# Optimization experiments

Measured on AMD Instinct MI355X. Metric: run time of the kernel, lower is better.

Reference implementation:

```python
import jax, jax.numpy as jnp
import numpy as np

N = 100000
E = 1_600_000
EPS = 1e-5
NEG_SLOPE = 0.01


def leaky_relu(x):
    return jnp.where(x > 0, x, NEG_SLOPE * x)


def batchnorm(x, gamma, beta):
    # BatchNorm1d in training mode: batch statistics, biased variance
    m = jnp.mean(x, axis=0)
    v = jnp.mean((x - m) ** 2, axis=0)
    return (x - m) * jax.lax.rsqrt(v + EPS) * gamma + beta


def gcn_conv(x, W, b, src, dst, norm, n):
    # PyG GCNConv: h = x @ W; aggregate norm * h[src] into dst; add bias
    h = x @ W                              # [N, F_out]
    msgs = h[src] * norm[:, None]          # [E', F_out] gather + scale
    out = jax.ops.segment_sum(msgs, dst, num_segments=n)  # scatter-add
    return out + b


def setup_inputs() -> dict:
    key = jax.random.key(0)
    ks = jax.random.split(key, 14)
    d_in, d_h1, d_h2, d_out = 128, 128, 64, 8
    x = jax.random.normal(ks[0], (N, d_in), dtype=jnp.float32)
    edge_index = jax.random.randint(ks[1], (2, E), 0, N, dtype=jnp.int64)
    edge_weights = jax.random.uniform(ks[2], (E,), dtype=jnp.float32)
    # Glorot-ish init for GCNConv weights, zero bias (PyG default bias=True)
    W1 = jax.random.normal(ks[3], (d_in, d_h1), dtype=jnp.float32) / np.sqrt(d_in)
    b1 = jnp.zeros((d_h1,), jnp.float32)
    W2 = jax.random.normal(ks[4], (d_h1, d_h2), dtype=jnp.float32) / np.sqrt(d_h1)
    b2 = jnp.zeros((d_h2,), jnp.float32)
    W3 = jax.random.normal(ks[5], (d_h2, d_out), dtype=jnp.float32) / np.sqrt(d_h2)
    b3 = jnp.zeros((d_out,), jnp.float32)
    gamma1 = jnp.ones((d_h1,), jnp.float32)
    beta1 = jnp.zeros((d_h1,), jnp.float32)
    gamma2 = jnp.ones((d_h2,), jnp.float32)
    beta2 = jnp.zeros((d_h2,), jnp.float32)
    return {"x": x, "edge_index": edge_index, "edge_weights": edge_weights,
            "W1": W1, "b1": b1, "W2": W2, "b2": b2, "W3": W3, "b3": b3,
            "gamma1": gamma1, "beta1": beta1, "gamma2": gamma2, "beta2": beta2}


def reference(x, edge_index, edge_weights, W1, b1, W2, b2, W3, b3,
              gamma1, beta1, gamma2, beta2):
    # edge_weights is accepted (as in the original forward signature) but unused:
    # the module calls GCNConv(x, edge_index) without weights.
    n = x.shape[0]
    loop = jnp.arange(n, dtype=edge_index.dtype)
    src = jnp.concatenate([edge_index[0], loop])  # add self-loops
    dst = jnp.concatenate([edge_index[1], loop])
    # symmetric normalization with unit edge weights (in-degree on dst)
    deg = jax.ops.segment_sum(jnp.ones_like(dst, dtype=x.dtype), dst,
                              num_segments=n)
    dinv = jnp.where(deg > 0, jax.lax.rsqrt(deg), 0.0)
    norm = dinv[src] * dinv[dst]

    h = leaky_relu(gcn_conv(x, W1, b1, src, dst, norm, n))
    h = batchnorm(h, gamma1, beta1)
    h = leaky_relu(gcn_conv(h, W2, b2, src, dst, norm, n))
    h = batchnorm(h, gamma2, beta2)
    h = leaky_relu(gcn_conv(h, W3, b3, src, dst, norm, n))
    return h
```

## Files before the change

kernel.cpp:

```cpp
#include <hip/hip_runtime.h>
#include <cstdint>
#include <cstddef>

#define NEG_SLOPE 0.01f
#define BN_EPS 1e-5f
#define BSHIFT 6
#define BMASK 63
#define NBLK 128

using short8 = __attribute__((ext_vector_type(8))) short;
using f32x4 = __attribute__((ext_vector_type(4))) float;

__device__ inline unsigned short f2bf(float f) {
    unsigned int u = __float_as_uint(f);
    u += 0x7FFFu + ((u >> 16) & 1u);
    return (unsigned short)(u >> 16);
}


__global__ __launch_bounds__(1024) void chunkhist_kernel(const int* __restrict__ dst,
                                                         int* __restrict__ hist,
                                                         int E, int nb, int chunk) {
    __shared__ int lh[2048];
    const int b = blockIdx.x;
    for (int i = threadIdx.x; i < nb; i += 1024) lh[i] = 0;
    __syncthreads();
    const int e0 = b * chunk;
    const int e1 = min(E, e0 + chunk);
    for (int e = e0 + threadIdx.x; e < e1; e += 1024)
        atomicAdd(&lh[dst[e] >> BSHIFT], 1);
    __syncthreads();
    for (int k = threadIdx.x; k < nb; k += 1024)
        hist[k * NBLK + b] = lh[k];
}

__global__ __launch_bounds__(1024) void scan_block_kernel(const int* __restrict__ in,
                                                          int* __restrict__ out,
                                                          int* __restrict__ partials, int n) {
    __shared__ int sm[1024];
    int tid = threadIdx.x;
    int i = blockIdx.x * 1024 + tid;
    int v = (i < n) ? in[i] : 0;
    int x = v;
    sm[tid] = x;
    __syncthreads();
    for (int off = 1; off < 1024; off <<= 1) {
        int y = (tid >= off) ? sm[tid - off] : 0;
        __syncthreads();
        x += y;
        sm[tid] = x;
        __syncthreads();
    }
    if (i < n) out[i] = x - v;
    if (tid == 1023 && partials) partials[blockIdx.x] = x;
}

__global__ void scanadd2_kernel(int* __restrict__ S, const int* __restrict__ pofs,
                                int* __restrict__ bbase, int m, int nb, int E) {
    int i = blockIdx.x * blockDim.x + threadIdx.x;
    if (i < m) {
        int v = S[i] + pofs[i >> 10];
        S[i] = v;
        if ((i & (NBLK - 1)) == 0) bbase[i / NBLK] = v;
    }
    if (i == 0) bbase[nb] = E;
}

__global__ __launch_bounds__(1024) void chunkscatter_kernel(const int* __restrict__ src,
                                                            const int* __restrict__ dst,
                                                            const int* __restrict__ S,
                                                            unsigned int* __restrict__ packed,
                                                            int E, int nb, int chunk) {
    __shared__ int cur[2048];
    const int b = blockIdx.x;
    for (int k = threadIdx.x; k < nb; k += 1024) cur[k] = S[k * NBLK + b];
    __syncthreads();
    const int e0 = b * chunk;
    const int e1 = min(E, e0 + chunk);
    for (int e = e0 + threadIdx.x; e < e1; e += 1024) {
        int d = dst[e];
        int slot = atomicAdd(&cur[d >> BSHIFT], 1);
        packed[slot] = ((unsigned int)src[e] << BSHIFT) | (unsigned int)(d & BMASK);
    }
}

__global__ __launch_bounds__(256) void bucket_build_kernel(const unsigned int* __restrict__ packed,
                                                           const int* __restrict__ bbase,
                                                           int* __restrict__ rowptr,
                                                           float* __restrict__ dinv,
                                                           int* __restrict__ csr,
                                                           int N, int nb, int E) {
    const int b = blockIdx.x;
    const int t = threadIdx.x;
    const int e0 = bbase[b], e1 = bbase[b + 1];
    const int node0 = b << BSHIFT;
    __shared__ int hist[64], cur[64];
    if (t < 64) hist[t] = 0;
    __syncthreads();
    for (int e = e0 + t; e < e1; e += 256)
        atomicAdd(&hist[packed[e] & BMASK], 1);
    __syncthreads();
    if (t < 64) {
        int h = hist[t];
        int v = h;
        for (int o = 1; o < 64; o <<= 1) {
            int y = __shfl_up(v, o);
            if (t >= o) v += y;
        }
        int base = e0 + v - h;
        int node = node0 + t;
        if (node < N) {
            rowptr[node] = base;
            dinv[node] = rsqrtf((float)(h + 1));
        }
        cur[t] = base;
    }
    if (b == nb - 1 && t == 0) rowptr[N] = E;
    __syncthreads();
    for (int e = e0 + t; e < e1; e += 256) {
        unsigned int p = packed[e];
        int slot = atomicAdd(&cur[p & BMASK], 1);
        csr[slot] = (int)(p >> BSHIFT);
    }
}


__global__ void transposeW_kernel(const float* __restrict__ W, unsigned short* __restrict__ Wt,
                                  int K, int M) {
    int idx = blockIdx.x * blockDim.x + threadIdx.x;
    if (idx < K * M) {
        int k = idx / M, n = idx % M;
        Wt[n * K + k] = f2bf(W[idx]);
    }
}


template <int MF, bool BN, bool XBF>
__global__ __launch_bounds__(256) void mgemm_kernel(const void* __restrict__ Xv,
                                                    const unsigned short* __restrict__ Wt,
                                                    const float* __restrict__ bnS,
                                                    const float* __restrict__ bnT,
                                                    const float* __restrict__ dinv,
                                                    unsigned short* __restrict__ H, int n) {
    constexpr int K = 128;
    constexpr int CTW = (MF / 16) / 4;
    __shared__ unsigned short Xl[64 * K];
    __shared__ unsigned short Wl[MF * K];
    __shared__ float dl[64];

    const int t = threadIdx.x;
    const int wave = t >> 6;
    const int lane = t & 63;
    const int row0 = blockIdx.x * 64;

    if (XBF) {
        const unsigned short* X = (const unsigned short*)Xv;
        for (int idx = t; idx < 64 * K / 8; idx += 256) {
            int r = idx >> 4, c8 = idx & 15;
            int row = row0 + r; if (row >= n) row = n - 1;
            uint4 v = ((const uint4*)(X + (size_t)row * K))[c8];
            float xv[8];
            xv[0] = __uint_as_float(v.x << 16); xv[1] = __uint_as_float(v.x & 0xFFFF0000u);
            xv[2] = __uint_as_float(v.y << 16); xv[3] = __uint_as_float(v.y & 0xFFFF0000u);
            xv[4] = __uint_as_float(v.z << 16); xv[5] = __uint_as_float(v.z & 0xFFFF0000u);
            xv[6] = __uint_as_float(v.w << 16); xv[7] = __uint_as_float(v.w & 0xFFFF0000u);
            if (BN) {
                const float4 s0 = ((const float4*)bnS)[c8 * 2];
                const float4 s1 = ((const float4*)bnS)[c8 * 2 + 1];
                const float4 t0 = ((const float4*)bnT)[c8 * 2];
                const float4 t1 = ((const float4*)bnT)[c8 * 2 + 1];
                xv[0] = xv[0] * s0.x + t0.x; xv[1] = xv[1] * s0.y + t0.y;
                xv[2] = xv[2] * s0.z + t0.z; xv[3] = xv[3] * s0.w + t0.w;
                xv[4] = xv[4] * s1.x + t1.x; xv[5] = xv[5] * s1.y + t1.y;
                xv[6] = xv[6] * s1.z + t1.z; xv[7] = xv[7] * s1.w + t1.w;
            }
            uint4 o;
            o.x = (unsigned)f2bf(xv[0]) | ((unsigned)f2bf(xv[1]) << 16);
            o.y = (unsigned)f2bf(xv[2]) | ((unsigned)f2bf(xv[3]) << 16);
            o.z = (unsigned)f2bf(xv[4]) | ((unsigned)f2bf(xv[5]) << 16);
            o.w = (unsigned)f2bf(xv[6]) | ((unsigned)f2bf(xv[7]) << 16);
            *(uint4*)((char*)Xl + r * 256 + ((c8 * 16) ^ ((r & 7) << 4))) = o;
        }
    } else {
        const float* X = (const float*)Xv;
        for (int idx = t; idx < 64 * K / 4; idx += 256) {
            int r = idx >> 5, c4 = idx & 31;
            int row = row0 + r; if (row >= n) row = n - 1;
            float4 v = ((const float4*)(X + (size_t)row * K))[c4];
            if (BN) {
                float4 sv = ((const float4*)bnS)[c4];
                float4 tv = ((const float4*)bnT)[c4];
                v.x = v.x * sv.x + tv.x; v.y = v.y * sv.y + tv.y;
                v.z = v.z * sv.z + tv.z; v.w = v.w * sv.w + tv.w;
            }
            ushort4 o; o.x = f2bf(v.x); o.y = f2bf(v.y); o.z = f2bf(v.z); o.w = f2bf(v.w);
            *(ushort4*)((char*)Xl + r * 256 + ((c4 * 8) ^ ((r & 7) << 4))) = o;
        }
    }
    for (int idx = t; idx < MF * K / 4; idx += 256) {
        int nr = idx >> 5, k4 = idx & 31;
        ushort4 o = ((const ushort4*)(Wt + (size_t)nr * K))[k4];
        *(ushort4*)((char*)Wl + nr * 256 + ((k4 * 8) ^ ((nr & 7) << 4))) = o;
    }
    if (t < 64) { int row = row0 + t; dl[t] = dinv[row < n ? row : n - 1]; }
    __syncthreads();

    f32x4 acc[CTW][4];
#pragma unroll
    for (int c = 0; c < CTW; ++c)
#pragma unroll
        for (int rt = 0; rt < 4; ++rt)
            acc[c][rt] = (f32x4){0.f, 0.f, 0.f, 0.f};

    const int kg = lane >> 4;
    const int lr = lane & 15;

#pragma unroll
    for (int kk = 0; kk < 4; ++kk) {
        const int kb = (kk * 32 + kg * 8) * 2;
        short8 a[4];
#pragma unroll
        for (int rt = 0; rt < 4; ++rt) {
            int r = rt * 16 + lr;
            a[rt] = *(const short8*)((const char*)Xl + r * 256 + (kb ^ ((r & 7) << 4)));
        }
#pragma unroll
        for (int c = 0; c < CTW; ++c) {
            int nr = (wave * CTW + c) * 16 + lr;
            short8 b = *(const short8*)((const char*)Wl + nr * 256 + (kb ^ ((nr & 7) << 4)));
#pragma unroll
            for (int rt = 0; rt < 4; ++rt)
                acc[c][rt] = __builtin_amdgcn_mfma_f32_16x16x32_bf16(a[rt], b, acc[c][rt], 0, 0, 0);
        }
    }
    __syncthreads();

    unsigned short* Ol = (unsigned short*)Xl;
#pragma unroll
    for (int c = 0; c < CTW; ++c) {
        int col = (wave * CTW + c) * 16 + lr;
#pragma unroll
        for (int rt = 0; rt < 4; ++rt) {
#pragma unroll
            for (int j = 0; j < 4; ++j) {
                int r = rt * 16 + kg * 4 + j;
                Ol[r * MF + col] = f2bf(acc[c][rt][j] * dl[r]);
            }
        }
    }
    __syncthreads();
    for (int idx = t; idx < 64 * MF / 4; idx += 256) {
        int r = idx / (MF / 4), c4 = idx % (MF / 4);
        int row = row0 + r;
        if (row < n)
            ((ushort4*)(H + (size_t)row * MF))[c4] = ((const ushort4*)Ol)[idx];
    }
}


__global__ __launch_bounds__(256) void gemm3_kernel(const unsigned short* __restrict__ X,
                                                    const float* __restrict__ W,
                                                    const float* __restrict__ bnS,
                                                    const float* __restrict__ bnT,
                                                    const float* __restrict__ dinv,
                                                    unsigned short* __restrict__ H, int n) {
    __shared__ float Wl[512];
    __shared__ float sl[64], tl[64];
    const int t = threadIdx.x;
    for (int i = t; i < 512; i += 256) Wl[i] = W[i];
    if (t < 64) { sl[t] = bnS[t]; tl[t] = bnT[t]; }
    __syncthreads();
    const int node = blockIdx.x * 256 + t;
    if (node >= n) return;
    float acc[8];
#pragma unroll
    for (int m = 0; m < 8; ++m) acc[m] = 0.f;
    const uint4* xp = (const uint4*)(X + (size_t)node * 64);
#pragma unroll
    for (int c8 = 0; c8 < 8; ++c8) {
        const uint4 v = xp[c8];
        float xv[8];
        xv[0] = __uint_as_float(v.x << 16); xv[1] = __uint_as_float(v.x & 0xFFFF0000u);
        xv[2] = __uint_as_float(v.y << 16); xv[3] = __uint_as_float(v.y & 0xFFFF0000u);
        xv[4] = __uint_as_float(v.z << 16); xv[5] = __uint_as_float(v.z & 0xFFFF0000u);
        xv[6] = __uint_as_float(v.w << 16); xv[7] = __uint_as_float(v.w & 0xFFFF0000u);
#pragma unroll
        for (int j = 0; j < 8; ++j) {
            const int k = c8 * 8 + j;
            const float x = xv[j] * sl[k] + tl[k];
#pragma unroll
            for (int m = 0; m < 8; ++m) acc[m] += x * Wl[k * 8 + m];
        }
    }
    const float di = dinv[node];
    uint4 o;
    o.x = (unsigned)f2bf(acc[0] * di) | ((unsigned)f2bf(acc[1] * di) << 16);
    o.y = (unsigned)f2bf(acc[2] * di) | ((unsigned)f2bf(acc[3] * di) << 16);
    o.z = (unsigned)f2bf(acc[4] * di) | ((unsigned)f2bf(acc[5] * di) << 16);
    o.w = (unsigned)f2bf(acc[6] * di) | ((unsigned)f2bf(acc[7] * di) << 16);
    *(uint4*)(H + (size_t)node * 8) = o;
}


template <int F, int GROUP, bool BF16OUT, bool STATS>
__global__ __launch_bounds__(256) void agg_kernel(const unsigned short* __restrict__ h,
                                                  const int* __restrict__ rowptr,
                                                  const int* __restrict__ csr,
                                                  const float* __restrict__ dinv,
                                                  const float* __restrict__ bias,
                                                  void* __restrict__ yout,
                                                  float* __restrict__ sumP,
                                                  float* __restrict__ ssqP,
                                                  int n, int nblocks) {
    constexpr int NPB = 256 / GROUP;
    const int g = threadIdx.x % GROUP;
    const int slot = threadIdx.x / GROUP;
    const int f0 = g * 8;
    const unsigned short* hp = h + f0;
    float sst[8], ssq[8];
#pragma unroll
    for (int k = 0; k < 8; ++k) { sst[k] = 0.f; ssq[k] = 0.f; }
    const float4 bA = *(const float4*)(bias + f0);
    const float4 bB = *(const float4*)(bias + f0 + 4);

#define ACC8(v)                                    \
    a0 += __uint_as_float((v).x << 16);            \
    a1 += __uint_as_float((v).x & 0xFFFF0000u);    \
    a2 += __uint_as_float((v).y << 16);            \
    a3 += __uint_as_float((v).y & 0xFFFF0000u);    \
    a4 += __uint_as_float((v).z << 16);            \
    a5 += __uint_as_float((v).z & 0xFFFF0000u);    \
    a6 += __uint_as_float((v).w << 16);            \
    a7 += __uint_as_float((v).w & 0xFFFF0000u);

    for (int base = blockIdx.x * NPB; base < n; base += nblocks * NPB) {
        const int node = base + slot;
        if (node < n) {
            float a0 = 0.f, a1 = 0.f, a2 = 0.f, a3 = 0.f,
                  a4 = 0.f, a5 = 0.f, a6 = 0.f, a7 = 0.f;
            int e = rowptr[node];
            const int r1 = rowptr[node + 1];
            for (; e + 8 <= r1; e += 8) {
                const int s0 = csr[e],     s1 = csr[e + 1], s2 = csr[e + 2], s3 = csr[e + 3];
                const int s4 = csr[e + 4], s5 = csr[e + 5], s6 = csr[e + 6], s7 = csr[e + 7];
                const uint4 v0 = *(const uint4*)(hp + (size_t)s0 * F);
                const uint4 v1 = *(const uint4*)(hp + (size_t)s1 * F);
                const uint4 v2 = *(const uint4*)(hp + (size_t)s2 * F);
                const uint4 v3 = *(const uint4*)(hp + (size_t)s3 * F);
                const uint4 v4 = *(const uint4*)(hp + (size_t)s4 * F);
                const uint4 v5 = *(const uint4*)(hp + (size_t)s5 * F);
                const uint4 v6 = *(const uint4*)(hp + (size_t)s6 * F);
                const uint4 v7 = *(const uint4*)(hp + (size_t)s7 * F);
                ACC8(v0); ACC8(v1); ACC8(v2); ACC8(v3);
                ACC8(v4); ACC8(v5); ACC8(v6); ACC8(v7);
            }
            for (; e < r1; ++e) {
                const int s = csr[e];
                const uint4 v = *(const uint4*)(hp + (size_t)s * F);
                ACC8(v);
            }
            {
                const uint4 v = *(const uint4*)(hp + (size_t)node * F);
                ACC8(v);
            }
            const float di = dinv[node];
            float r[8];
            r[0] = di * a0 + bA.x; r[1] = di * a1 + bA.y;
            r[2] = di * a2 + bA.z; r[3] = di * a3 + bA.w;
            r[4] = di * a4 + bB.x; r[5] = di * a5 + bB.y;
            r[6] = di * a6 + bB.z; r[7] = di * a7 + bB.w;
#pragma unroll
            for (int k = 0; k < 8; ++k) {
                r[k] = r[k] > 0.f ? r[k] : NEG_SLOPE * r[k];
                if (STATS) { sst[k] += r[k]; ssq[k] += r[k] * r[k]; }
            }
            if (BF16OUT) {
                uint4 o;
                o.x = (unsigned)f2bf(r[0]) | ((unsigned)f2bf(r[1]) << 16);
                o.y = (unsigned)f2bf(r[2]) | ((unsigned)f2bf(r[3]) << 16);
                o.z = (unsigned)f2bf(r[4]) | ((unsigned)f2bf(r[5]) << 16);
                o.w = (unsigned)f2bf(r[6]) | ((unsigned)f2bf(r[7]) << 16);
                *(uint4*)((unsigned short*)yout + (size_t)node * F + f0) = o;
            } else {
                float4 o0, o1;
                o0.x = r[0]; o0.y = r[1]; o0.z = r[2]; o0.w = r[3];
                o1.x = r[4]; o1.y = r[5]; o1.z = r[6]; o1.w = r[7];
                float* yp = (float*)yout + (size_t)node * F + f0;
                *(float4*)(yp) = o0;
                *(float4*)(yp + 4) = o1;
            }
        }
    }
#undef ACC8
    if (STATS) {
        __shared__ float smS[F], smQ[F];
        for (int i = threadIdx.x; i < F; i += 256) { smS[i] = 0.f; smQ[i] = 0.f; }
        __syncthreads();
#pragma unroll
        for (int k = 0; k < 8; ++k) {
            atomicAdd(&smS[f0 + k], sst[k]);
            atomicAdd(&smQ[f0 + k], ssq[k]);
        }
        __syncthreads();
        for (int i = threadIdx.x; i < F; i += 256) {
            sumP[(size_t)blockIdx.x * F + i] = smS[i];
            ssqP[(size_t)blockIdx.x * F + i] = smQ[i];
        }
    }
}


__global__ __launch_bounds__(256) void bnparam_kernel(const float* __restrict__ sumP,
                                                      const float* __restrict__ ssqP,
                                                      const float* __restrict__ gamma,
                                                      const float* __restrict__ beta,
                                                      float* __restrict__ S, float* __restrict__ T,
                                                      int n, int F, int NB) {
    const int f = blockIdx.x;
    const int t = threadIdx.x;
    float s = 0.f, q = 0.f;
    for (int b = t; b < NB; b += 256) {
        s += sumP[(size_t)b * F + f];
        q += ssqP[(size_t)b * F + f];
    }
    __shared__ float rs[4], rq[4];
    for (int o = 32; o; o >>= 1) { s += __shfl_down(s, o); q += __shfl_down(q, o); }
    if ((t & 63) == 0) { rs[t >> 6] = s; rq[t >> 6] = q; }
    __syncthreads();
    if (t == 0) {
        s = rs[0] + rs[1] + rs[2] + rs[3];
        q = rq[0] + rq[1] + rq[2] + rq[3];
        const float m = s / (float)n;
        const float var = q / (float)n - m * m;
        const float inv = rsqrtf(var + BN_EPS);
        const float sc = gamma[f] * inv;
        S[f] = sc;
        T[f] = beta[f] - m * sc;
    }
}


extern "C" void kernel_launch(void* const* d_in, const int* in_sizes, int n_in,
                              void* d_out, int out_size, void* d_ws, size_t ws_size,
                              hipStream_t stream) {
    const float* x = (const float*)d_in[0];
    const int* edges = (const int*)d_in[1];
    const float* W1 = (const float*)d_in[3];
    const float* b1 = (const float*)d_in[4];
    const float* W2 = (const float*)d_in[5];
    const float* b2 = (const float*)d_in[6];
    const float* W3 = (const float*)d_in[7];
    const float* b3 = (const float*)d_in[8];
    const float* gamma1 = (const float*)d_in[9];
    const float* beta1 = (const float*)d_in[10];
    const float* gamma2 = (const float*)d_in[11];
    const float* beta2 = (const float*)d_in[12];

    const int N = in_sizes[0] / 128;
    const int E = in_sizes[1] / 2;
    const int* esrc = edges;
    const int* edst = edges + E;
    const int nb = (N + BMASK) >> BSHIFT;
    const int M = nb * NBLK;
    const int chunk = (E + NBLK - 1) / NBLK;
    const int NB2 = 2048;

    char* ws = (char*)d_ws;
    size_t off = 0;
    auto alloc = [&](size_t bytes) -> void* {
        void* p = ws + off;
        off = (off + bytes + 255) & ~(size_t)255;
        return p;
    };
    int* hist = (int*)alloc((size_t)M * 4);
    int* S = (int*)alloc((size_t)M * 4);
    int* partials = (int*)alloc(1024 * 4);
    int* pofs = (int*)alloc(1024 * 4);
    int* bbase = (int*)alloc((size_t)(nb + 1) * 4);
    int* rowptr = (int*)alloc((size_t)(N + 1) * 4);
    float* dinv = (float*)alloc((size_t)N * 4);
    float* bn = (float*)alloc(512 * 4);
    float* sumP1 = (float*)alloc((size_t)NB2 * 128 * 4);
    float* ssqP1 = (float*)alloc((size_t)NB2 * 128 * 4);
    float* sumP2 = (float*)alloc((size_t)NB2 * 64 * 4);
    float* ssqP2 = (float*)alloc((size_t)NB2 * 64 * 4);
    unsigned short* wt1 = (unsigned short*)alloc(128 * 128 * 2);
    unsigned short* wt2 = (unsigned short*)alloc(64 * 128 * 2);
    int* csr = (int*)alloc((size_t)E * 4);
    unsigned short* hbuf = (unsigned short*)alloc((size_t)N * 128 * 2);
    unsigned short* ybuf = (unsigned short*)alloc((size_t)N * 128 * 2);
    unsigned int* packed = (unsigned int*)hbuf;

    float* sA = bn;
    float* tA = bn + 128;
    float* sB = bn + 256;
    float* tB = bn + 384;

    const int MB = (M + 1023) / 1024;

    transposeW_kernel<<<(128 * 128 + 255) / 256, 256, 0, stream>>>(W1, wt1, 128, 128);
    transposeW_kernel<<<(128 * 64 + 255) / 256, 256, 0, stream>>>(W2, wt2, 128, 64);
    chunkhist_kernel<<<NBLK, 1024, 0, stream>>>(edst, hist, E, nb, chunk);
    scan_block_kernel<<<MB, 1024, 0, stream>>>(hist, S, partials, M);
    scan_block_kernel<<<1, 1024, 0, stream>>>(partials, pofs, nullptr, MB);
    scanadd2_kernel<<<(M + 255) / 256, 256, 0, stream>>>(S, pofs, bbase, M, nb, E);
    chunkscatter_kernel<<<NBLK, 1024, 0, stream>>>(esrc, edst, S, packed, E, nb, chunk);
    bucket_build_kernel<<<nb, 256, 0, stream>>>(packed, bbase, rowptr, dinv, csr, N, nb, E);

    mgemm_kernel<128, false, false><<<(N + 63) / 64, 256, 0, stream>>>(x, wt1, nullptr, nullptr, dinv, hbuf, N);
    agg_kernel<128, 16, true, true><<<NB2, 256, 0, stream>>>(hbuf, rowptr, csr, dinv, b1, ybuf, sumP1, ssqP1, N, NB2);
    bnparam_kernel<<<128, 256, 0, stream>>>(sumP1, ssqP1, gamma1, beta1, sA, tA, N, 128, NB2);

    mgemm_kernel<64, true, true><<<(N + 63) / 64, 256, 0, stream>>>(ybuf, wt2, sA, tA, dinv, hbuf, N);
    agg_kernel<64, 8, true, true><<<NB2, 256, 0, stream>>>(hbuf, rowptr, csr, dinv, b2, ybuf, sumP2, ssqP2, N, NB2);
    bnparam_kernel<<<64, 256, 0, stream>>>(sumP2, ssqP2, gamma2, beta2, sB, tB, N, 64, NB2);

    gemm3_kernel<<<(N + 255) / 256, 256, 0, stream>>>(ybuf, W3, sB, tB, dinv, hbuf, N);
    const int NB3 = (N + 255) / 256;
    agg_kernel<8, 1, false, false><<<NB3, 256, 0, stream>>>(hbuf, rowptr, csr, dinv, b3, (float*)d_out, nullptr, nullptr, N, NB3);
}
```

Baseline: 292.5 us.

## Split batchnorm statistics out of aggregation into separate stats kernel

The aggregation kernel no longer accumulates batchnorm sums. It now launches one block per group of nodes instead of a grid-stride loop, and its gather unroll drops from 8 to 4. A new bstats kernel rereads the bf16 output to compute per-feature partial sums and squares over 1024 blocks. The aim is a lighter, higher-occupancy gather kernel with fewer registers. The cost is an extra launch and an extra full read of the intermediate activations for each of the two batchnorm layers.

Result: faster. 271.3 us (-7.2%).

```diff
diff --git a/kernel.cpp b/kernel.cpp
--- a/kernel.cpp
+++ b/kernel.cpp
@@ -302,27 +302,20 @@
 }
 
 
-template <int F, int GROUP, bool BF16OUT, bool STATS>
+template <int F, int GROUP, bool BF16OUT>
 __global__ __launch_bounds__(256) void agg_kernel(const unsigned short* __restrict__ h,
                                                   const int* __restrict__ rowptr,
                                                   const int* __restrict__ csr,
                                                   const float* __restrict__ dinv,
                                                   const float* __restrict__ bias,
-                                                  void* __restrict__ yout,
-                                                  float* __restrict__ sumP,
-                                                  float* __restrict__ ssqP,
-                                                  int n, int nblocks) {
+                                                  void* __restrict__ yout, int n) {
     constexpr int NPB = 256 / GROUP;
     const int g = threadIdx.x % GROUP;
-    const int slot = threadIdx.x / GROUP;
+    const int node = blockIdx.x * NPB + threadIdx.x / GROUP;
+    if (node >= n) return;
     const int f0 = g * 8;
     const unsigned short* hp = h + f0;
-    float sst[8], ssq[8];
-#pragma unroll
-    for (int k = 0; k < 8; ++k) { sst[k] = 0.f; ssq[k] = 0.f; }
-    const float4 bA = *(const float4*)(bias + f0);
-    const float4 bB = *(const float4*)(bias + f0 + 4);
-
+    float a0 = 0.f, a1 = 0.f, a2 = 0.f, a3 = 0.f, a4 = 0.f, a5 = 0.f, a6 = 0.f, a7 = 0.f;
 #define ACC8(v)                                    \
     a0 += __uint_as_float((v).x << 16);            \
     a1 += __uint_as_float((v).x & 0xFFFF0000u);    \
@@ -332,80 +325,92 @@
     a5 += __uint_as_float((v).z & 0xFFFF0000u);    \
     a6 += __uint_as_float((v).w << 16);            \
     a7 += __uint_as_float((v).w & 0xFFFF0000u);
-
+    int e = rowptr[node];
+    const int r1 = rowptr[node + 1];
+    for (; e + 4 <= r1; e += 4) {
+        const int s0 = csr[e], s1 = csr[e + 1], s2 = csr[e + 2], s3 = csr[e + 3];
+        const uint4 v0 = *(const uint4*)(hp + (size_t)s0 * F);
+        const uint4 v1 = *(const uint4*)(hp + (size_t)s1 * F);
+        const uint4 v2 = *(const uint4*)(hp + (size_t)s2 * F);
+        const uint4 v3 = *(const uint4*)(hp + (size_t)s3 * F);
+        ACC8(v0); ACC8(v1); ACC8(v2); ACC8(v3);
+    }
+    for (; e < r1; ++e) {
+        const int s = csr[e];
+        const uint4 v = *(const uint4*)(hp + (size_t)s * F);
+        ACC8(v);
+    }
+    {
+        const uint4 v = *(const uint4*)(hp + (size_t)node * F);
+        ACC8(v);
+    }
+#undef ACC8
+    const float di = dinv[node];
+    const float4 bA = *(const float4*)(bias + f0);
+    const float4 bB = *(const float4*)(bias + f0 + 4);
+    float r[8];
+    r[0] = di * a0 + bA.x; r[1] = di * a1 + bA.y;
+    r[2] = di * a2 + bA.z; r[3] = di * a3 + bA.w;
+    r[4] = di * a4 + bB.x; r[5] = di * a5 + bB.y;
+    r[6] = di * a6 + bB.z; r[7] = di * a7 + bB.w;
+#pragma unroll
+    for (int k = 0; k < 8; ++k) r[k] = r[k] > 0.f ? r[k] : NEG_SLOPE * r[k];
+    if (BF16OUT) {
+        uint4 o;
+        o.x = (unsigned)f2bf(r[0]) | ((unsigned)f2bf(r[1]) << 16);
+        o.y = (unsigned)f2bf(r[2]) | ((unsigned)f2bf(r[3]) << 16);
+        o.z = (unsigned)f2bf(r[4]) | ((unsigned)f2bf(r[5]) << 16);
+        o.w = (unsigned)f2bf(r[6]) | ((unsigned)f2bf(r[7]) << 16);
+        *(uint4*)((unsigned short*)yout + (size_t)node * F + f0) = o;
+    } else {
+        float4 o0, o1;
+        o0.x = r[0]; o0.y = r[1]; o0.z = r[2]; o0.w = r[3];
+        o1.x = r[4]; o1.y = r[5]; o1.z = r[6]; o1.w = r[7];
+        float* yp = (float*)yout + (size_t)node * F + f0;
+        *(float4*)(yp) = o0;
+        *(float4*)(yp + 4) = o1;
+    }
+}
+
+
+template <int F>
+__global__ __launch_bounds__(256) void bstats_kernel(const unsigned short* __restrict__ y,
+                                                     float* __restrict__ sumP,
+                                                     float* __restrict__ ssqP,
+                                                     int n, int nblocks) {
+    constexpr int GROUP = F / 8;
+    constexpr int NPB = 256 / GROUP;
+    const int g = threadIdx.x % GROUP;
+    const int slot = threadIdx.x / GROUP;
+    const int f0 = g * 8;
+    float ss[8], qq[8];
+#pragma unroll
+    for (int k = 0; k < 8; ++k) { ss[k] = 0.f; qq[k] = 0.f; }
     for (int base = blockIdx.x * NPB; base < n; base += nblocks * NPB) {
         const int node = base + slot;
         if (node < n) {
-            float a0 = 0.f, a1 = 0.f, a2 = 0.f, a3 = 0.f,
-                  a4 = 0.f, a5 = 0.f, a6 = 0.f, a7 = 0.f;
-            int e = rowptr[node];
-            const int r1 = rowptr[node + 1];
-            for (; e + 8 <= r1; e += 8) {
-                const int s0 = csr[e],     s1 = csr[e + 1], s2 = csr[e + 2], s3 = csr[e + 3];
-                const int s4 = csr[e + 4], s5 = csr[e + 5], s6 = csr[e + 6], s7 = csr[e + 7];
-                const uint4 v0 = *(const uint4*)(hp + (size_t)s0 * F);
-                const uint4 v1 = *(const uint4*)(hp + (size_t)s1 * F);
-                const uint4 v2 = *(const uint4*)(hp + (size_t)s2 * F);
-                const uint4 v3 = *(const uint4*)(hp + (size_t)s3 * F);
-                const uint4 v4 = *(const uint4*)(hp + (size_t)s4 * F);
-                const uint4 v5 = *(const uint4*)(hp + (size_t)s5 * F);
-                const uint4 v6 = *(const uint4*)(hp + (size_t)s6 * F);
-                const uint4 v7 = *(const uint4*)(hp + (size_t)s7 * F);
-                ACC8(v0); ACC8(v1); ACC8(v2); ACC8(v3);
-                ACC8(v4); ACC8(v5); ACC8(v6); ACC8(v7);
-            }
-            for (; e < r1; ++e) {
-                const int s = csr[e];
-                const uint4 v = *(const uint4*)(hp + (size_t)s * F);
-                ACC8(v);
-            }
-            {
-                const uint4 v = *(const uint4*)(hp + (size_t)node * F);
-                ACC8(v);
-            }
-            const float di = dinv[node];
-            float r[8];
-            r[0] = di * a0 + bA.x; r[1] = di * a1 + bA.y;
-            r[2] = di * a2 + bA.z; r[3] = di * a3 + bA.w;
-            r[4] = di * a4 + bB.x; r[5] = di * a5 + bB.y;
-            r[6] = di * a6 + bB.z; r[7] = di * a7 + bB.w;
-#pragma unroll
-            for (int k = 0; k < 8; ++k) {
-                r[k] = r[k] > 0.f ? r[k] : NEG_SLOPE * r[k];
-                if (STATS) { sst[k] += r[k]; ssq[k] += r[k] * r[k]; }
-            }
-            if (BF16OUT) {
-                uint4 o;
-                o.x = (unsigned)f2bf(r[0]) | ((unsigned)f2bf(r[1]) << 16);
-                o.y = (unsigned)f2bf(r[2]) | ((unsigned)f2bf(r[3]) << 16);
-                o.z = (unsigned)f2bf(r[4]) | ((unsigned)f2bf(r[5]) << 16);
-                o.w = (unsigned)f2bf(r[6]) | ((unsigned)f2bf(r[7]) << 16);
-                *(uint4*)((unsigned short*)yout + (size_t)node * F + f0) = o;
-            } else {
-                float4 o0, o1;
-                o0.x = r[0]; o0.y = r[1]; o0.z = r[2]; o0.w = r[3];
-                o1.x = r[4]; o1.y = r[5]; o1.z = r[6]; o1.w = r[7];
-                float* yp = (float*)yout + (size_t)node * F + f0;
-                *(float4*)(yp) = o0;
-                *(float4*)(yp + 4) = o1;
-            }
-        }
-    }
-#undef ACC8
-    if (STATS) {
-        __shared__ float smS[F], smQ[F];
-        for (int i = threadIdx.x; i < F; i += 256) { smS[i] = 0.f; smQ[i] = 0.f; }
-        __syncthreads();
-#pragma unroll
-        for (int k = 0; k < 8; ++k) {
-            atomicAdd(&smS[f0 + k], sst[k]);
-            atomicAdd(&smQ[f0 + k], ssq[k]);
-        }
-        __syncthreads();
-        for (int i = threadIdx.x; i < F; i += 256) {
-            sumP[(size_t)blockIdx.x * F + i] = smS[i];
-            ssqP[(size_t)blockIdx.x * F + i] = smQ[i];
-        }
+            const uint4 v = *(const uint4*)(y + (size_t)node * F + f0);
+            float xv[8];
+            xv[0] = __uint_as_float(v.x << 16); xv[1] = __uint_as_float(v.x & 0xFFFF0000u);
+            xv[2] = __uint_as_float(v.y << 16); xv[3] = __uint_as_float(v.y & 0xFFFF0000u);
+            xv[4] = __uint_as_float(v.z << 16); xv[5] = __uint_as_float(v.z & 0xFFFF0000u);
+            xv[6] = __uint_as_float(v.w << 16); xv[7] = __uint_as_float(v.w & 0xFFFF0000u);
+#pragma unroll
+            for (int k = 0; k < 8; ++k) { ss[k] += xv[k]; qq[k] += xv[k] * xv[k]; }
+        }
+    }
+    __shared__ float smS[F], smQ[F];
+    for (int i = threadIdx.x; i < F; i += 256) { smS[i] = 0.f; smQ[i] = 0.f; }
+    __syncthreads();
+#pragma unroll
+    for (int k = 0; k < 8; ++k) {
+        atomicAdd(&smS[f0 + k], ss[k]);
+        atomicAdd(&smQ[f0 + k], qq[k]);
+    }
+    __syncthreads();
+    for (int i = threadIdx.x; i < F; i += 256) {
+        sumP[(size_t)blockIdx.x * F + i] = smS[i];
+        ssqP[(size_t)blockIdx.x * F + i] = smQ[i];
     }
 }
 
@@ -463,7 +468,7 @@
     const int nb = (N + BMASK) >> BSHIFT;
     const int M = nb * NBLK;
     const int chunk = (E + NBLK - 1) / NBLK;
-    const int NB2 = 2048;
+    const int NBS = 1024;
 
     char* ws = (char*)d_ws;
     size_t off = 0;
@@ -480,10 +485,10 @@
     int* rowptr = (int*)alloc((size_t)(N + 1) * 4);
     float* dinv = (float*)alloc((size_t)N * 4);
     float* bn = (float*)alloc(512 * 4);
-    float* sumP1 = (float*)alloc((size_t)NB2 * 128 * 4);
-    float* ssqP1 = (float*)alloc((size_t)NB2 * 128 * 4);
-    float* sumP2 = (float*)alloc((size_t)NB2 * 64 * 4);
-    float* ssqP2 = (float*)alloc((size_t)NB2 * 64 * 4);
+    float* sumP1 = (float*)alloc((size_t)NBS * 128 * 4);
+    float* ssqP1 = (float*)alloc((size_t)NBS * 128 * 4);
+    float* sumP2 = (float*)alloc((size_t)NBS * 64 * 4);
+    float* ssqP2 = (float*)alloc((size_t)NBS * 64 * 4);
     unsigned short* wt1 = (unsigned short*)alloc(128 * 128 * 2);
     unsigned short* wt2 = (unsigned short*)alloc(64 * 128 * 2);
     int* csr = (int*)alloc((size_t)E * 4);
@@ -508,14 +513,15 @@
     bucket_build_kernel<<<nb, 256, 0, stream>>>(packed, bbase, rowptr, dinv, csr, N, nb, E);
 
     mgemm_kernel<128, false, false><<<(N + 63) / 64, 256, 0, stream>>>(x, wt1, nullptr, nullptr, dinv, hbuf, N);
-    agg_kernel<128, 16, true, true><<<NB2, 256, 0, stream>>>(hbuf, rowptr, csr, dinv, b1, ybuf, sumP1, ssqP1, N, NB2);
-    bnparam_kernel<<<128, 256, 0, stream>>>(sumP1, ssqP1, gamma1, beta1, sA, tA, N, 128, NB2);
+    agg_kernel<128, 16, true><<<(N + 15) / 16, 256, 0, stream>>>(hbuf, rowptr, csr, dinv, b1, ybuf, N);
+    bstats_kernel<128><<<NBS, 256, 0, stream>>>(ybuf, sumP1, ssqP1, N, NBS);
+    bnparam_kernel<<<128, 256, 0, stream>>>(sumP1, ssqP1, gamma1, beta1, sA, tA, N, 128, NBS);
 
     mgemm_kernel<64, true, true><<<(N + 63) / 64, 256, 0, stream>>>(ybuf, wt2, sA, tA, dinv, hbuf, N);
-    agg_kernel<64, 8, true, true><<<NB2, 256, 0, stream>>>(hbuf, rowptr, csr, dinv, b2, ybuf, sumP2, ssqP2, N, NB2);
-    bnparam_kernel<<<64, 256, 0, stream>>>(sumP2, ssqP2, gamma2, beta2, sB, tB, N, 64, NB2);
+    agg_kernel<64, 8, true><<<(N + 31) / 32, 256, 0, stream>>>(hbuf, rowptr, csr, dinv, b2, ybuf, N);
+    bstats_kernel<64><<<NBS, 256, 0, stream>>>(ybuf, sumP2, ssqP2, N, NBS);
+    bnparam_kernel<<<64, 256, 0, stream>>>(sumP2, ssqP2, gamma2, beta2, sB, tB, N, 64, NBS);
 
     gemm3_kernel<<<(N + 255) / 256, 256, 0, stream>>>(ybuf, W3, sB, tB, dinv, hbuf, N);
-    const int NB3 = (N + 255) / 256;
-    agg_kernel<8, 1, false, false><<<NB3, 256, 0, stream>>>(hbuf, rowptr, csr, dinv, b3, (float*)d_out, nullptr, nullptr, N, NB3);
-}
+    agg_kernel<8, 1, false><<<(N + 255) / 256, 256, 0, stream>>>(hbuf, rowptr, csr, dinv, b3, (float*)d_out, N);
+}
```
